# Kernel tuning notes

Hardware: AMD Instinct MI355X
Metric: run time of the kernel (lower is better)

## Reference

```python
import jax, jax.numpy as jnp
import numpy as np

L, B, T, E, NH, HD, HID, V = 8, 2, 2048, 1024, 16, 64, 2816, 32000


def _rmsnorm(x, w, eps=1e-6):
    return w * (x * jax.lax.rsqrt(jnp.mean(x * x, axis=-1, keepdims=True) + eps))


def _rope(x, cos, sin):
    # x: [B,H,T,D]; cos/sin: [1,1,T,D/2]
    x1, x2 = jnp.split(x, 2, axis=-1)
    return jnp.concatenate([x1 * cos - x2 * sin, x1 * sin + x2 * cos], axis=-1)


def setup_inputs() -> dict:
    key = jax.random.key(0)
    ks = jax.random.split(key, 7)
    s = 0.02
    return {
        "idx": jax.random.randint(ks[0], (B, T), 0, V),
        "tok_emb": jax.random.normal(ks[1], (V, E), dtype=jnp.float32) * s,
        "qkv_w": jax.random.normal(ks[2], (L, 3 * E, E), dtype=jnp.float32) * s,
        "proj_w": jax.random.normal(ks[3], (L, E, E), dtype=jnp.float32) * s,
        "w1": jax.random.normal(ks[4], (L, HID, E), dtype=jnp.float32) * s,
        "w2": jax.random.normal(ks[5], (L, HID, E), dtype=jnp.float32) * s,
        "w3": jax.random.normal(ks[6], (L, E, HID), dtype=jnp.float32) * s,
        "norm1_w": jnp.ones((L, E), dtype=jnp.float32),
        "norm2_w": jnp.ones((L, E), dtype=jnp.float32),
        "norm_f_w": jnp.ones((E,), dtype=jnp.float32),
    }


def reference(idx, tok_emb, qkv_w, proj_w, w1, w2, w3, norm1_w, norm2_w, norm_f_w):
    x = tok_emb[idx]  # [B,T,E]
    # RoPE cache (start_pos=0, no kv cache -> prefill path)
    half = HD // 2
    inv_freq = 1.0 / (10000.0 ** (jnp.arange(half, dtype=jnp.float32) / half))
    pos = jnp.arange(T, dtype=jnp.float32)
    freqs = pos[:, None] * inv_freq[None, :]  # [T, D/2]
    cos = jnp.cos(freqs)[None, None]
    sin = jnp.sin(freqs)[None, None]
    causal = jnp.tril(jnp.ones((T, T), dtype=bool))
    scale = 1.0 / np.sqrt(HD).astype(np.float32)

    for l in range(L):
        # attention block
        h = _rmsnorm(x, norm1_w[l])
        qkv = h @ qkv_w[l].T  # [B,T,3E]
        q, k, v = jnp.split(qkv, 3, axis=-1)
        q = q.reshape(B, T, NH, HD).transpose(0, 2, 1, 3)
        k = k.reshape(B, T, NH, HD).transpose(0, 2, 1, 3)
        v = v.reshape(B, T, NH, HD).transpose(0, 2, 1, 3)
        q = _rope(q, cos, sin)
        k = _rope(k, cos, sin)
        att = jnp.einsum('bhqd,bhkd->bhqk', q, k) * scale
        att = jnp.where(causal, att, -jnp.inf)
        att = jax.nn.softmax(att, axis=-1)
        o = jnp.einsum('bhqk,bhkd->bhqd', att, v)
        o = o.transpose(0, 2, 1, 3).reshape(B, T, E)
        x = x + o @ proj_w[l].T
        # SwiGLU MLP
        h = _rmsnorm(x, norm2_w[l])
        x = x + (jax.nn.silu(h @ w1[l].T) * (h @ w2[l].T)) @ w3[l].T

    x = _rmsnorm(x, norm_f_w)
    logits = x @ tok_emb.T  # tied lm_head
    return logits
```

## Files before the change

### kernel.cpp

```cpp
#include <hip/hip_runtime.h>

#define GLOBAL_AS __attribute__((address_space(1)))
#define LDS_AS __attribute__((address_space(3)))

typedef unsigned short u16;
typedef unsigned int u32;
typedef __attribute__((ext_vector_type(4))) float f32x4;
typedef __attribute__((ext_vector_type(8))) short bf16x8;

#define TT 2048
#define EE 1024
#define NHH 16
#define HDD 64
#define HIDD 2816
#define VV 32000
#define MM 4096

__device__ __forceinline__ u16 f2bf(float f) {
  u32 u = __builtin_bit_cast(u32, f);
  u += 0x7fffu + ((u >> 16) & 1u);
  return (u16)(u >> 16);
}
__device__ __forceinline__ float bf2f(u16 v) {
  return __builtin_bit_cast(float, (u32)v << 16);
}


__global__ __launch_bounds__(256) void castbf_k(const float* __restrict__ in,
                                                u16* __restrict__ o, long n4) {
  const long i = (long)blockIdx.x * 256 + threadIdx.x;
  if (i >= n4) return;
  const float4 v = ((const float4*)in)[i];
  ((uint2*)o)[i] = make_uint2((u32)f2bf(v.x) | ((u32)f2bf(v.y) << 16),
                              (u32)f2bf(v.z) | ((u32)f2bf(v.w) << 16));
}

__global__ void ropetab_k(float* __restrict__ cosT, float* __restrict__ sinT) {
  const int t = blockIdx.x, j = threadIdx.x;
  const float inv = powf(10000.0f, -(float)j * (1.0f / 32.0f));
  const float f = (float)t * inv;
  cosT[t * 32 + j] = cosf(f);
  sinT[t * 32 + j] = sinf(f);
}

__global__ __launch_bounds__(256) void embed_k(const int* __restrict__ idx,
                                               const float* __restrict__ temb,
                                               float* __restrict__ x) {
  const int row = blockIdx.x;
  const int id = idx[row];
  ((float4*)(x + (size_t)row * EE))[threadIdx.x] =
      ((const float4*)(temb + (size_t)id * EE))[threadIdx.x];
}

__global__ __launch_bounds__(256) void rmsnorm_k(const float* __restrict__ x,
                                                 const float* __restrict__ w,
                                                 u16* __restrict__ o) {
  __shared__ float red[4];
  const int row = blockIdx.x, tid = threadIdx.x;
  const float4 v = ((const float4*)(x + (size_t)row * EE))[tid];
  float ss = v.x * v.x + v.y * v.y + v.z * v.z + v.w * v.w;
#pragma unroll
  for (int off = 32; off; off >>= 1) ss += __shfl_xor(ss, off, 64);
  if ((tid & 63) == 0) red[tid >> 6] = ss;
  __syncthreads();
  const float inv = rsqrtf((red[0] + red[1] + red[2] + red[3]) * (1.0f / 1024.0f) + 1e-6f);
  const float4 wv = ((const float4*)w)[tid];
  const u32 lo = (u32)f2bf(v.x * inv * wv.x) | ((u32)f2bf(v.y * inv * wv.y) << 16);
  const u32 hi = (u32)f2bf(v.z * inv * wv.z) | ((u32)f2bf(v.w * inv * wv.w) << 16);
  ((uint2*)(o + (size_t)row * EE))[tid] = make_uint2(lo, hi);
}

template <int OUTBF>
__global__ __launch_bounds__(512, 2) void gemm256p(const u16* __restrict__ A,
                                                   const u16* __restrict__ Bw,
                                                   float* __restrict__ C,
                                                   u16* __restrict__ C16,
                                                   const u16* __restrict__ G,
                                                   const float* __restrict__ cosT,
                                                   const float* __restrict__ sinT,
                                                   u16* __restrict__ Qb,
                                                   u16* __restrict__ Kb,
                                                   u16* __restrict__ Vtb,
                                                   int N, int K) {
  __shared__ u16 lds[2 * 32768];
  const int t = threadIdx.x;
  const int lane = t & 63;
  const int wid = t >> 6;
  const int wr = wid >> 2;
  const int wc = wid & 3;
  const int l15 = lane & 15, lg = lane >> 4;
  const int bid = blockIdx.x;
  const int row0 = (bid & 15) << 8;
  const int col0 = (bid >> 4) << 8;
  const int NT = K >> 6;

  const int sr = t >> 3;
  const int su8 = (((t & 7) ^ (sr & 7)) << 3);
  const int t8 = t << 3;
  const u16* aG[4];
#pragma unroll
  for (int ga = 0; ga < 4; ++ga)
    aG[ga] = A + (size_t)(row0 + ga * 64 + sr) * K + su8;
  const u16* bG[4];
#pragma unroll
  for (int gb = 0; gb < 4; ++gb) {
    const int q = (gb * 2 + (sr >> 5)) & 3;
    const int nh = gb >> 1;
    bG[gb] = Bw + (size_t)(col0 + q * 64 + nh * 32 + (sr & 31)) * K + su8;
  }

  const int u0 = ((lg ^ (l15 & 7)) << 3);
  const int u1 = (((4 | lg) ^ (l15 & 7)) << 3);
  const int arow = (wr * 128 + l15) << 6;
  const int brow = 16384 + ((wc * 32 + l15) << 6);

  f32x4 acc[8][4] = {};

#define STA(nb, ga, k0n)                                                              \
  __builtin_amdgcn_global_load_lds((const GLOBAL_AS void*)(aG[ga] + (k0n)),           \
                                   (LDS_AS void*)((nb) + (ga)*4096 + t8), 16, 0, 0)
#define STB(nb, gb, k0n)                                                              \
  __builtin_amdgcn_global_load_lds((const GLOBAL_AS void*)(bG[gb] + (k0n)),           \
                                   (LDS_AS void*)((nb) + 16384 + (gb)*4096 + t8), 16, 0, 0)

  {
    u16* nb = lds;
    STA(nb, 0, 0); STA(nb, 2, 0);
    STB(nb, 0, 0); STB(nb, 1, 0);
    STB(nb, 2, 0); STB(nb, 3, 0);
    STA(nb, 1, 0); STA(nb, 3, 0);
  }

  bf16x8 af[4][2], bl[2][2], bh[2][2];

  for (int kt = 0; kt < NT; ++kt) {
    const bool st = (kt + 1 < NT);
    const int k0n = (kt + 1) << 6;
    const u16* cb = lds + (kt & 1) * 32768;
    u16* nb = lds + ((kt + 1) & 1) * 32768;

    asm volatile("s_waitcnt vmcnt(4)" ::: "memory");
    __builtin_amdgcn_s_barrier();
#pragma unroll
    for (int mi = 0; mi < 4; ++mi) {
      af[mi][0] = *(const bf16x8*)&cb[arow + mi * 1024 + u0];
      af[mi][1] = *(const bf16x8*)&cb[arow + mi * 1024 + u1];
    }
#pragma unroll
    for (int ni = 0; ni < 2; ++ni) {
      bl[ni][0] = *(const bf16x8*)&cb[brow + ni * 1024 + u0];
      bl[ni][1] = *(const bf16x8*)&cb[brow + ni * 1024 + u1];
    }
    if (st) { STA(nb, 0, k0n); STA(nb, 2, k0n); }
    __builtin_amdgcn_s_setprio(1);
#pragma unroll
    for (int mi = 0; mi < 4; ++mi)
#pragma unroll
      for (int ni = 0; ni < 2; ++ni) {
        acc[mi][ni] = __builtin_amdgcn_mfma_f32_16x16x32_bf16(af[mi][0], bl[ni][0], acc[mi][ni], 0, 0, 0);
        acc[mi][ni] = __builtin_amdgcn_mfma_f32_16x16x32_bf16(af[mi][1], bl[ni][1], acc[mi][ni], 0, 0, 0);
      }
    __builtin_amdgcn_s_setprio(0);

    if (st) { asm volatile("s_waitcnt vmcnt(4)" ::: "memory"); }
    else    { asm volatile("s_waitcnt vmcnt(2)" ::: "memory"); }
    __builtin_amdgcn_s_barrier();
#pragma unroll
    for (int ni = 0; ni < 2; ++ni) {
      bh[ni][0] = *(const bf16x8*)&cb[brow + 8192 + ni * 1024 + u0];
      bh[ni][1] = *(const bf16x8*)&cb[brow + 8192 + ni * 1024 + u1];
    }
    if (st) { STB(nb, 0, k0n); STB(nb, 1, k0n); }
    __builtin_amdgcn_s_setprio(1);
#pragma unroll
    for (int mi = 0; mi < 4; ++mi)
#pragma unroll
      for (int ni = 0; ni < 2; ++ni) {
        acc[mi][2 + ni] = __builtin_amdgcn_mfma_f32_16x16x32_bf16(af[mi][0], bh[ni][0], acc[mi][2 + ni], 0, 0, 0);
        acc[mi][2 + ni] = __builtin_amdgcn_mfma_f32_16x16x32_bf16(af[mi][1], bh[ni][1], acc[mi][2 + ni], 0, 0, 0);
      }
    __builtin_amdgcn_s_setprio(0);

    if (st) { asm volatile("s_waitcnt vmcnt(4)" ::: "memory"); }
    else    { asm volatile("s_waitcnt vmcnt(0)" ::: "memory"); }
    __builtin_amdgcn_s_barrier();
#pragma unroll
    for (int mi = 0; mi < 4; ++mi) {
      af[mi][0] = *(const bf16x8*)&cb[arow + (4 + mi) * 1024 + u0];
      af[mi][1] = *(const bf16x8*)&cb[arow + (4 + mi) * 1024 + u1];
    }
    if (st) { STB(nb, 2, k0n); STB(nb, 3, k0n); }
    __builtin_amdgcn_s_setprio(1);
#pragma unroll
    for (int mi = 0; mi < 4; ++mi)
#pragma unroll
      for (int ni = 0; ni < 2; ++ni) {
        acc[4 + mi][2 + ni] = __builtin_amdgcn_mfma_f32_16x16x32_bf16(af[mi][0], bh[ni][0], acc[4 + mi][2 + ni], 0, 0, 0);
        acc[4 + mi][2 + ni] = __builtin_amdgcn_mfma_f32_16x16x32_bf16(af[mi][1], bh[ni][1], acc[4 + mi][2 + ni], 0, 0, 0);
      }
    __builtin_amdgcn_s_setprio(0);

    if (st) { STA(nb, 1, k0n); STA(nb, 3, k0n); }
    __builtin_amdgcn_s_setprio(1);
#pragma unroll
    for (int mi = 0; mi < 4; ++mi)
#pragma unroll
      for (int ni = 0; ni < 2; ++ni) {
        acc[4 + mi][ni] = __builtin_amdgcn_mfma_f32_16x16x32_bf16(af[mi][0], bl[ni][0], acc[4 + mi][ni], 0, 0, 0);
        acc[4 + mi][ni] = __builtin_amdgcn_mfma_f32_16x16x32_bf16(af[mi][1], bl[ni][1], acc[4 + mi][ni], 0, 0, 0);
      }
    __builtin_amdgcn_s_setprio(0);
  }
#undef STA
#undef STB

  if (OUTBF == 3) {
    const int reg = col0 >> 10;
    const int fb = col0 & 1023;
#pragma unroll
    for (int m = 0; m < 8; ++m) {
      const int row = row0 + wr * 128 + m * 16 + lg * 4;
      const int b = row >> 11, tbase = row & 2047;
      if (reg < 2) {
        u16* dstp = (reg == 0) ? Qb : Kb;
        const float qs = (reg == 0) ? 0.125f : 1.0f;
#pragma unroll
        for (int n = 0; n < 2; ++n) {
          const int f = fb + wc * 64 + n * 16 + l15;
          const int h = f >> 6, j = f & 63;
#pragma unroll
          for (int r = 0; r < 4; ++r) {
            const int tt = tbase + r;
            const float c = cosT[tt * 32 + j], s = sinT[tt * 32 + j];
            const float x1 = acc[m][n][r], x2 = acc[m][n | 2][r];
            const size_t ro = ((size_t)(b * NHH + h) * TT + tt) * HDD + j;
            dstp[ro] = f2bf((x1 * c - x2 * s) * qs);
            dstp[ro + 32] = f2bf((x1 * s + x2 * c) * qs);
          }
        }
      } else {
#pragma unroll
        for (int n = 0; n < 4; ++n) {
          const int f = fb + wc * 64 + n * 16 + l15;
          const int h = f >> 6, j = f & 63;
          ushort4 pk;
          pk.x = f2bf(acc[m][n][0]);
          pk.y = f2bf(acc[m][n][1]);
          pk.z = f2bf(acc[m][n][2]);
          pk.w = f2bf(acc[m][n][3]);
          *(ushort4*)&Vtb[((size_t)(b * NHH + h) * HDD + j) * TT + tbase] = pk;
        }
      }
    }
    return;
  }

#pragma unroll
  for (int m = 0; m < 8; ++m) {
    const int row = row0 + wr * 128 + m * 16 + lg * 4;
#pragma unroll
    for (int n = 0; n < 4; ++n) {
      const int col = col0 + wc * 64 + n * 16 + l15;
#pragma unroll
      for (int r = 0; r < 4; ++r) {
        const size_t o = (size_t)(row + r) * N + col;
        if (OUTBF == 0) {
          C[o] = acc[m][n][r];
        } else if (OUTBF == 1) {
          C16[o] = f2bf(acc[m][n][r]);
        } else {
          const float g = bf2f(G[o]);
          C16[o] = f2bf(g / (1.0f + __expf(-g)) * acc[m][n][r]);
        }
      }
    }
  }
}

__global__ __launch_bounds__(512, 2) void gemm128r(const u16* __restrict__ A,
                                                   const u16* __restrict__ Bw,
                                                   float* __restrict__ C,
                                                   const float* __restrict__ R,
                                                   int N, int K) {
  __shared__ u16 lds[4 * 8192];
  const int t = threadIdx.x;
  const int lane = t & 63;
  const int wid = t >> 6;
  const int wr = wid >> 2;
  const int wc = wid & 3;
  const int l15 = lane & 15, lg = lane >> 4;
  const int bid = blockIdx.x;
  const int row0 = (bid & 31) << 7;
  const int col0 = (bid >> 5) << 7;
  const int NT = K >> 5;

  const int rA = t >> 2;
  const int usw = (((t & 3) ^ ((t >> 3) & 3)) << 3);
  const u16* sA = A + (size_t)(row0 + rA) * K + usw;
  const u16* sB = Bw + (size_t)(col0 + rA) * K + usw;
  const int dst = t << 3;

  const int e8 = ((lg ^ ((l15 >> 1) & 3)) << 3);
  const int aoff = (wr * 64 + l15) * 32 + e8;
  const int boff = 4096 + (wc * 32 + l15) * 32 + e8;

  f32x4 acc[4][2] = {};

  auto stage = [&](int kt) {
    u16* base = &lds[(kt & 3) * 8192];
    const size_t ko = (size_t)kt * 32;
    __builtin_amdgcn_global_load_lds((const GLOBAL_AS void*)(sA + ko),
                                     (LDS_AS void*)(base + dst), 16, 0, 0);
    __builtin_amdgcn_global_load_lds((const GLOBAL_AS void*)(sB + ko),
                                     (LDS_AS void*)(base + 4096 + dst), 16, 0, 0);
  };

  stage(0);
  stage(1);
  stage(2);

  for (int kt = 0; kt < NT; ++kt) {
    const int rem = NT - 1 - kt;
    if (rem >= 2) {
      asm volatile("s_waitcnt vmcnt(4)" ::: "memory");
    } else if (rem == 1) {
      asm volatile("s_waitcnt vmcnt(2)" ::: "memory");
    } else {
      asm volatile("s_waitcnt vmcnt(0)" ::: "memory");
    }
    __builtin_amdgcn_s_barrier();
    if (kt + 3 < NT) stage(kt + 3);
    const u16* base = &lds[(kt & 3) * 8192];
    bf16x8 af[4], bfv[2];
#pragma unroll
    for (int m = 0; m < 4; ++m) af[m] = *(const bf16x8*)&base[aoff + m * 512];
#pragma unroll
    for (int n = 0; n < 2; ++n) bfv[n] = *(const bf16x8*)&base[boff + n * 512];
    __builtin_amdgcn_s_setprio(1);
#pragma unroll
    for (int m = 0; m < 4; ++m)
#pragma unroll
      for (int n = 0; n < 2; ++n)
        acc[m][n] = __builtin_amdgcn_mfma_f32_16x16x32_bf16(af[m], bfv[n], acc[m][n], 0, 0, 0);
    __builtin_amdgcn_s_setprio(0);
  }

#pragma unroll
  for (int m = 0; m < 4; ++m) {
    const int row = row0 + wr * 64 + m * 16 + lg * 4;
#pragma unroll
    for (int n = 0; n < 2; ++n) {
      const int col = col0 + wc * 32 + n * 16 + l15;
#pragma unroll
      for (int r = 0; r < 4; ++r) {
        const size_t o = (size_t)(row + r) * N + col;
        C[o] = acc[m][n][r] + R[o];
      }
    }
  }
}

__global__ __launch_bounds__(256) void attn_k(const u16* __restrict__ Q,
                                              const u16* __restrict__ Kc,
                                              const u16* __restrict__ Vt,
                                              u16* __restrict__ O) {
  __shared__ u16 P_lds[4][32][72];
  const int bh = blockIdx.y;
  const int q0 = blockIdx.x * 128;
  const int lane = threadIdx.x & 63;
  const int w = threadIdx.x >> 6;
  const int l15 = lane & 15, lg = lane >> 4;
  const int qbase = q0 + w * 32;

  bf16x8 qf[2][2];
#pragma unroll
  for (int am = 0; am < 2; ++am)
#pragma unroll
    for (int ks = 0; ks < 2; ++ks)
      qf[am][ks] = *(const bf16x8*)&Q[((size_t)bh * TT + qbase + am * 16 + l15) * HDD + ks * 32 + lg * 8];

  bf16x8 ones;
#pragma unroll
  for (int i = 0; i < 8; ++i) ones[i] = (short)0x3F80;

  f32x4 oacc[2][4] = {};
  f32x4 lacc[2] = {};

  const int ntile = (q0 + 128) >> 6;
  for (int kt = 0; kt < ntile; ++kt) {
    const int k0 = kt << 6;
    f32x4 s[2][4];
    bf16x8 kf0[4], kf1[4];
#pragma unroll
    for (int an = 0; an < 4; ++an) {
      kf0[an] = *(const bf16x8*)&Kc[((size_t)bh * TT + k0 + an * 16 + l15) * HDD + lg * 8];
      kf1[an] = *(const bf16x8*)&Kc[((size_t)bh * TT + k0 + an * 16 + l15) * HDD + 32 + lg * 8];
    }
    __builtin_amdgcn_s_setprio(1);
#pragma unroll
    for (int an = 0; an < 4; ++an) {
#pragma unroll
      for (int am = 0; am < 2; ++am) {
        f32x4 z = {0.0f, 0.0f, 0.0f, 0.0f};
        z = __builtin_amdgcn_mfma_f32_16x16x32_bf16(qf[am][0], kf0[an], z, 0, 0, 0);
        s[am][an] = __builtin_amdgcn_mfma_f32_16x16x32_bf16(qf[am][1], kf1[an], z, 0, 0, 0);
      }
    }
    __builtin_amdgcn_s_setprio(0);
    const bool diag = (k0 + 64) > q0;
#pragma unroll
    for (int am = 0; am < 2; ++am)
#pragma unroll
      for (int an = 0; an < 4; ++an)
#pragma unroll
        for (int r = 0; r < 4; ++r) {
          float v = s[am][an][r];
          if (diag) {
            const int qrow = qbase + am * 16 + lg * 4 + r;
            const int kcol = k0 + an * 16 + l15;
            if (kcol > qrow) v = -1e30f;
          }
          s[am][an][r] = __expf(v);
        }
#pragma unroll
    for (int am = 0; am < 2; ++am)
#pragma unroll
      for (int an = 0; an < 4; ++an)
#pragma unroll
        for (int r = 0; r < 4; ++r)
          P_lds[w][am * 16 + lg * 4 + r][an * 16 + l15] = f2bf(s[am][an][r]);
#pragma unroll
    for (int ks = 0; ks < 2; ++ks) {
      bf16x8 pf[2];
#pragma unroll
      for (int am = 0; am < 2; ++am)
        pf[am] = *(const bf16x8*)&P_lds[w][am * 16 + l15][ks * 32 + lg * 8];
      __builtin_amdgcn_s_setprio(1);
#pragma unroll
      for (int dn = 0; dn < 4; ++dn) {
        const bf16x8 vf = *(const bf16x8*)&Vt[((size_t)bh * HDD + dn * 16 + l15) * TT + k0 + ks * 32 + lg * 8];
#pragma unroll
        for (int am = 0; am < 2; ++am)
          oacc[am][dn] = __builtin_amdgcn_mfma_f32_16x16x32_bf16(pf[am], vf, oacc[am][dn], 0, 0, 0);
      }
#pragma unroll
      for (int am = 0; am < 2; ++am)
        lacc[am] = __builtin_amdgcn_mfma_f32_16x16x32_bf16(pf[am], ones, lacc[am], 0, 0, 0);
      __builtin_amdgcn_s_setprio(0);
    }
  }
  const int b = bh >> 4, h = bh & 15;
#pragma unroll
  for (int am = 0; am < 2; ++am)
#pragma unroll
    for (int r = 0; r < 4; ++r) {
      const float il = 1.0f / lacc[am][r];
      const int qrow = qbase + am * 16 + lg * 4 + r;
#pragma unroll
      for (int dn = 0; dn < 4; ++dn)
        O[((size_t)b * TT + qrow) * EE + h * 64 + dn * 16 + l15] = f2bf(oacc[am][dn][r] * il);
    }
}


extern "C" void kernel_launch(void* const* d_in, const int* in_sizes, int n_in,
                              void* d_out, int out_size, void* d_ws, size_t ws_size,
                              hipStream_t stream) {
  const int* idx = (const int*)d_in[0];
  const float* tok_emb = (const float*)d_in[1];
  const float* qkv_w = (const float*)d_in[2];
  const float* proj_w = (const float*)d_in[3];
  const float* w1 = (const float*)d_in[4];
  const float* w2 = (const float*)d_in[5];
  const float* w3 = (const float*)d_in[6];
  const float* norm1_w = (const float*)d_in[7];
  const float* norm2_w = (const float*)d_in[8];
  const float* norm_f_w = (const float*)d_in[9];
  float* out = (float*)d_out;

  char* ws = (char*)d_ws;
  size_t off = 0;
  auto alloc = [&](size_t bytes) -> void* {
    off = (off + 255) & ~(size_t)255;
    void* p = ws + off;
    off += bytes;
    return p;
  };

  const size_t N_TEMB = (size_t)VV * EE;
  const size_t N_QKVW = (size_t)8 * 3 * EE * EE;
  const size_t N_PROJW = (size_t)8 * EE * EE;
  const size_t N_W1 = (size_t)8 * HIDD * EE;
  const size_t N_W3 = (size_t)8 * EE * HIDD;

  u16* tembbf = (u16*)alloc(N_TEMB * 2);
  u16* qkvwbf = (u16*)alloc(N_QKVW * 2);
  u16* projwbf = (u16*)alloc(N_PROJW * 2);
  u16* w1bf = (u16*)alloc(N_W1 * 2);
  u16* w2bf = (u16*)alloc(N_W1 * 2);
  u16* w3bf = (u16*)alloc(N_W3 * 2);
  float* x = (float*)alloc((size_t)MM * EE * 4);
  u16* h1 = (u16*)alloc((size_t)MM * EE * 2);
  u16* hg = (u16*)alloc((size_t)MM * HIDD * 2);
  u16* qb = (u16*)alloc((size_t)2 * NHH * TT * HDD * 2);
  u16* kb = (u16*)alloc((size_t)2 * NHH * TT * HDD * 2);
  u16* vtb = (u16*)alloc((size_t)2 * NHH * TT * HDD * 2);
  u16* attno = (u16*)alloc((size_t)MM * EE * 2);
  float* cosT = (float*)alloc((size_t)TT * 32 * 4);
  float* sinT = (float*)alloc((size_t)TT * 32 * 4);

  u16* g16 = (u16*)(out + 16777216);

  auto cast = [&](const float* src, u16* dst, size_t n) {
    const long n4 = (long)(n / 4);
    castbf_k<<<(int)((n4 + 255) / 256), 256, 0, stream>>>(src, dst, n4);
  };
  cast(tok_emb, tembbf, N_TEMB);
  cast(qkv_w, qkvwbf, N_QKVW);
  cast(proj_w, projwbf, N_PROJW);
  cast(w1, w1bf, N_W1);
  cast(w2, w2bf, N_W1);
  cast(w3, w3bf, N_W3);

  ropetab_k<<<TT, 32, 0, stream>>>(cosT, sinT);
  embed_k<<<MM, 256, 0, stream>>>(idx, tok_emb, x);

  for (int l = 0; l < 8; ++l) {
    rmsnorm_k<<<MM, 256, 0, stream>>>(x, norm1_w + l * EE, h1);
    gemm256p<3><<<dim3(12 * 16), 512, 0, stream>>>(h1, qkvwbf + (size_t)l * 3 * EE * EE,
                                                   nullptr, nullptr, nullptr,
                                                   cosT, sinT, qb, kb, vtb, 3 * EE, EE);
    attn_k<<<dim3(16, 32), 256, 0, stream>>>(qb, kb, vtb, attno);
    gemm128r<<<dim3(8 * 32), 512, 0, stream>>>(attno, projwbf + (size_t)l * EE * EE,
                                               x, x, EE, EE);
    rmsnorm_k<<<MM, 256, 0, stream>>>(x, norm2_w + l * EE, h1);
    gemm256p<1><<<dim3(11 * 16), 512, 0, stream>>>(h1, w1bf + (size_t)l * HIDD * EE,
                                                   nullptr, g16, nullptr,
                                                   nullptr, nullptr, nullptr, nullptr, nullptr,
                                                   HIDD, EE);
    gemm256p<2><<<dim3(11 * 16), 512, 0, stream>>>(h1, w2bf + (size_t)l * HIDD * EE,
                                                   nullptr, hg, g16,
                                                   nullptr, nullptr, nullptr, nullptr, nullptr,
                                                   HIDD, EE);
    gemm128r<<<dim3(8 * 32), 512, 0, stream>>>(hg, w3bf + (size_t)l * EE * HIDD,
                                               x, x, EE, HIDD);
  }
  rmsnorm_k<<<MM, 256, 0, stream>>>(x, norm_f_w, h1);
  gemm256p<0><<<dim3(125 * 16), 512, 0, stream>>>(h1, tembbf, out, nullptr, nullptr,
                                                  nullptr, nullptr, nullptr, nullptr, nullptr,
                                                  VV, EE);
}
```

Baseline: 2.741 ms.

## Move QKV and MLP GEMMs to 128x128 tiles and reorder attention blocks

Replaces the 256x256-tile GEMM for the QKV, w1 and w2 projections with a templated 128x128-tile kernel that carries the RoPE, SiLU-gate and residual epilogues, so these launches get many more workgroups (768/704 instead of 192/176). The proj and w3 residual GEMMs use the same kernel with a transposed wave layout. Attention becomes a 1D grid that pairs long and short causal query blocks, which should balance load across CUs. In exchange, smaller tiles lower arithmetic intensity and reuse per workgroup.

New measurement: 2.568 ms. 1.07x faster.

```diff
diff --git a/kernel.cpp b/kernel.cpp
--- a/kernel.cpp
+++ b/kernel.cpp
@@ -76,11 +76,6 @@
                                                    float* __restrict__ C,
                                                    u16* __restrict__ C16,
                                                    const u16* __restrict__ G,
-                                                   const float* __restrict__ cosT,
-                                                   const float* __restrict__ sinT,
-                                                   u16* __restrict__ Qb,
-                                                   u16* __restrict__ Kb,
-                                                   u16* __restrict__ Vtb,
                                                    int N, int K) {
   __shared__ u16 lds[2 * 32768];
   const int t = threadIdx.x;
@@ -214,12 +209,110 @@
 #undef STA
 #undef STB
 
+#pragma unroll
+  for (int m = 0; m < 8; ++m) {
+    const int row = row0 + wr * 128 + m * 16 + lg * 4;
+#pragma unroll
+    for (int n = 0; n < 4; ++n) {
+      const int col = col0 + wc * 64 + n * 16 + l15;
+#pragma unroll
+      for (int r = 0; r < 4; ++r) {
+        const size_t o = (size_t)(row + r) * N + col;
+        if (OUTBF == 0) {
+          C[o] = acc[m][n][r];
+        } else if (OUTBF == 1) {
+          C16[o] = f2bf(acc[m][n][r]);
+        } else {
+          const float g = bf2f(G[o]);
+          C16[o] = f2bf(g / (1.0f + __expf(-g)) * acc[m][n][r]);
+        }
+      }
+    }
+  }
+}
+
+template <int OUTBF>
+__global__ __launch_bounds__(512, 2) void gemm128n(const u16* __restrict__ A,
+                                                   const u16* __restrict__ Bw,
+                                                   float* __restrict__ C,
+                                                   const float* __restrict__ R,
+                                                   u16* __restrict__ C16,
+                                                   const u16* __restrict__ G,
+                                                   const float* __restrict__ cosT,
+                                                   const float* __restrict__ sinT,
+                                                   u16* __restrict__ Qb,
+                                                   u16* __restrict__ Kb,
+                                                   u16* __restrict__ Vtb,
+                                                   int N, int K) {
+  __shared__ u16 lds[4 * 8192];
+  const int t = threadIdx.x;
+  const int lane = t & 63;
+  const int wid = t >> 6;
+  const int wr = wid & 3;
+  const int wc = wid >> 2;
+  const int l15 = lane & 15, lg = lane >> 4;
+  const int bid = blockIdx.x;
+  const int row0 = (bid & 31) << 7;
+  const int col0 = (bid >> 5) << 7;
+  const int NT = K >> 5;
+
+  const int rA = t >> 2;
+  const int usw = (((t & 3) ^ ((t >> 3) & 3)) << 3);
+  const u16* sA = A + (size_t)(row0 + rA) * K + usw;
+  const u16* sB = Bw + (size_t)(col0 + rA) * K + usw;
+  const int dst = t << 3;
+
+  const int e8 = ((lg ^ ((l15 >> 1) & 3)) << 3);
+  const int aoff = (wr * 32 + l15) * 32 + e8;
+  const int boff = 4096 + (wc * 64 + l15) * 32 + e8;
+
+  f32x4 acc[2][4] = {};
+
+  auto stage = [&](int kt) {
+    u16* base = &lds[(kt & 3) * 8192];
+    const size_t ko = (size_t)kt * 32;
+    __builtin_amdgcn_global_load_lds((const GLOBAL_AS void*)(sA + ko),
+                                     (LDS_AS void*)(base + dst), 16, 0, 0);
+    __builtin_amdgcn_global_load_lds((const GLOBAL_AS void*)(sB + ko),
+                                     (LDS_AS void*)(base + 4096 + dst), 16, 0, 0);
+  };
+
+  stage(0);
+  stage(1);
+  stage(2);
+
+  for (int kt = 0; kt < NT; ++kt) {
+    const int rem = NT - 1 - kt;
+    if (rem >= 2) {
+      asm volatile("s_waitcnt vmcnt(4)" ::: "memory");
+    } else if (rem == 1) {
+      asm volatile("s_waitcnt vmcnt(2)" ::: "memory");
+    } else {
+      asm volatile("s_waitcnt vmcnt(0)" ::: "memory");
+    }
+    __builtin_amdgcn_s_barrier();
+    if (kt + 3 < NT) stage(kt + 3);
+    const u16* base = &lds[(kt & 3) * 8192];
+    bf16x8 af[2], bfv[4];
+#pragma unroll
+    for (int m = 0; m < 2; ++m) af[m] = *(const bf16x8*)&base[aoff + m * 512];
+#pragma unroll
+    for (int n = 0; n < 4; ++n) bfv[n] = *(const bf16x8*)&base[boff + n * 512];
+    __builtin_amdgcn_s_setprio(1);
+#pragma unroll
+    for (int m = 0; m < 2; ++m)
+#pragma unroll
+      for (int n = 0; n < 4; ++n)
+        acc[m][n] = __builtin_amdgcn_mfma_f32_16x16x32_bf16(af[m], bfv[n], acc[m][n], 0, 0, 0);
+    __builtin_amdgcn_s_setprio(0);
+  }
+
   if (OUTBF == 3) {
     const int reg = col0 >> 10;
     const int fb = col0 & 1023;
 #pragma unroll
-    for (int m = 0; m < 8; ++m) {
-      const int row = row0 + wr * 128 + m * 16 + lg * 4;
+    for (int m = 0; m < 2; ++m) {
+      const int row = row0 + wr * 32 + m * 16 + lg * 4;
       const int b = row >> 11, tbase = row & 2047;
       if (reg < 2) {
         u16* dstp = (reg == 0) ? Qb : Kb;
@@ -256,8 +349,8 @@
   }
 
 #pragma unroll
-  for (int m = 0; m < 8; ++m) {
-    const int row = row0 + wr * 128 + m * 16 + lg * 4;
+  for (int m = 0; m < 2; ++m) {
+    const int row = row0 + wr * 32 + m * 16 + lg * 4;
 #pragma unroll
     for (int n = 0; n < 4; ++n) {
       const int col = col0 + wc * 64 + n * 16 + l15;
@@ -265,7 +358,7 @@
       for (int r = 0; r < 4; ++r) {
         const size_t o = (size_t)(row + r) * N + col;
         if (OUTBF == 0) {
-          C[o] = acc[m][n][r];
+          C[o] = acc[m][n][r] + R[o];
         } else if (OUTBF == 1) {
           C16[o] = f2bf(acc[m][n][r]);
         } else {
@@ -277,96 +370,16 @@
   }
 }
 
-__global__ __launch_bounds__(512, 2) void gemm128r(const u16* __restrict__ A,
-                                                   const u16* __restrict__ Bw,
-                                                   float* __restrict__ C,
-                                                   const float* __restrict__ R,
-                                                   int N, int K) {
-  __shared__ u16 lds[4 * 8192];
-  const int t = threadIdx.x;
-  const int lane = t & 63;
-  const int wid = t >> 6;
-  const int wr = wid >> 2;
-  const int wc = wid & 3;
-  const int l15 = lane & 15, lg = lane >> 4;
-  const int bid = blockIdx.x;
-  const int row0 = (bid & 31) << 7;
-  const int col0 = (bid >> 5) << 7;
-  const int NT = K >> 5;
-
-  const int rA = t >> 2;
-  const int usw = (((t & 3) ^ ((t >> 3) & 3)) << 3);
-  const u16* sA = A + (size_t)(row0 + rA) * K + usw;
-  const u16* sB = Bw + (size_t)(col0 + rA) * K + usw;
-  const int dst = t << 3;
-
-  const int e8 = ((lg ^ ((l15 >> 1) & 3)) << 3);
-  const int aoff = (wr * 64 + l15) * 32 + e8;
-  const int boff = 4096 + (wc * 32 + l15) * 32 + e8;
-
-  f32x4 acc[4][2] = {};
-
-  auto stage = [&](int kt) {
-    u16* base = &lds[(kt & 3) * 8192];
-    const size_t ko = (size_t)kt * 32;
-    __builtin_amdgcn_global_load_lds((const GLOBAL_AS void*)(sA + ko),
-                                     (LDS_AS void*)(base + dst), 16, 0, 0);
-    __builtin_amdgcn_global_load_lds((const GLOBAL_AS void*)(sB + ko),
-                                     (LDS_AS void*)(base + 4096 + dst), 16, 0, 0);
-  };
-
-  stage(0);
-  stage(1);
-  stage(2);
-
-  for (int kt = 0; kt < NT; ++kt) {
-    const int rem = NT - 1 - kt;
-    if (rem >= 2) {
-      asm volatile("s_waitcnt vmcnt(4)" ::: "memory");
-    } else if (rem == 1) {
-      asm volatile("s_waitcnt vmcnt(2)" ::: "memory");
-    } else {
-      asm volatile("s_waitcnt vmcnt(0)" ::: "memory");
-    }
-    __builtin_amdgcn_s_barrier();
-    if (kt + 3 < NT) stage(kt + 3);
-    const u16* base = &lds[(kt & 3) * 8192];
-    bf16x8 af[4], bfv[2];
-#pragma unroll
-    for (int m = 0; m < 4; ++m) af[m] = *(const bf16x8*)&base[aoff + m * 512];
-#pragma unroll
-    for (int n = 0; n < 2; ++n) bfv[n] = *(const bf16x8*)&base[boff + n * 512];
-    __builtin_amdgcn_s_setprio(1);
-#pragma unroll
-    for (int m = 0; m < 4; ++m)
-#pragma unroll
-      for (int n = 0; n < 2; ++n)
-        acc[m][n] = __builtin_amdgcn_mfma_f32_16x16x32_bf16(af[m], bfv[n], acc[m][n], 0, 0, 0);
-    __builtin_amdgcn_s_setprio(0);
-  }
-
-#pragma unroll
-  for (int m = 0; m < 4; ++m) {
-    const int row = row0 + wr * 64 + m * 16 + lg * 4;
-#pragma unroll
-    for (int n = 0; n < 2; ++n) {
-      const int col = col0 + wc * 32 + n * 16 + l15;
-#pragma unroll
-      for (int r = 0; r < 4; ++r) {
-        const size_t o = (size_t)(row + r) * N + col;
-        C[o] = acc[m][n][r] + R[o];
-      }
-    }
-  }
-}
-
 __global__ __launch_bounds__(256) void attn_k(const u16* __restrict__ Q,
                                               const u16* __restrict__ Kc,
                                               const u16* __restrict__ Vt,
                                               u16* __restrict__ O) {
   __shared__ u16 P_lds[4][32][72];
-  const int bh = blockIdx.y;
-  const int q0 = blockIdx.x * 128;
+  const int bid = blockIdx.x;
+  const int bh = bid & 31;
+  const int jj = bid >> 5;
+  const int qi = (bid < 256) ? jj : 23 - jj;
+  const int q0 = qi << 7;
   const int lane = threadIdx.x & 63;
   const int w = threadIdx.x >> 6;
   const int l15 = lane & 15, lg = lane >> 4;
@@ -527,26 +540,29 @@
 
   for (int l = 0; l < 8; ++l) {
     rmsnorm_k<<<MM, 256, 0, stream>>>(x, norm1_w + l * EE, h1);
-    gemm256p<3><<<dim3(12 * 16), 512, 0, stream>>>(h1, qkvwbf + (size_t)l * 3 * EE * EE,
-                                                   nullptr, nullptr, nullptr,
+    gemm128n<3><<<dim3(24 * 32), 512, 0, stream>>>(h1, qkvwbf + (size_t)l * 3 * EE * EE,
+                                                   nullptr, nullptr, nullptr, nullptr,
                                                    cosT, sinT, qb, kb, vtb, 3 * EE, EE);
-    attn_k<<<dim3(16, 32), 256, 0, stream>>>(qb, kb, vtb, attno);
-    gemm128r<<<dim3(8 * 32), 512, 0, stream>>>(attno, projwbf + (size_t)l * EE * EE,
-                                               x, x, EE, EE);
+    attn_k<<<dim3(512), 256, 0, stream>>>(qb, kb, vtb, attno);
+    gemm128n<0><<<dim3(8 * 32), 512, 0, stream>>>(attno, projwbf + (size_t)l * EE * EE,
+                                                  x, x, nullptr, nullptr,
+                                                  nullptr, nullptr, nullptr, nullptr, nullptr,
+                                                  EE, EE);
     rmsnorm_k<<<MM, 256, 0, stream>>>(x, norm2_w + l * EE, h1);
-    gemm256p<1><<<dim3(11 * 16), 512, 0, stream>>>(h1, w1bf + (size_t)l * HIDD * EE,
-                                                   nullptr, g16, nullptr,
+    gemm128n<1><<<dim3(22 * 32), 512, 0, stream>>>(h1, w1bf + (size_t)l * HIDD * EE,
+                                                   nullptr, nullptr, g16, nullptr,
                                                    nullptr, nullptr, nullptr, nullptr, nullptr,
                                                    HIDD, EE);
-    gemm256p<2><<<dim3(11 * 16), 512, 0, stream>>>(h1, w2bf + (size_t)l * HIDD * EE,
-                                                   nullptr, hg, g16,
+    gemm128n<2><<<dim3(22 * 32), 512, 0, stream>>>(h1, w2bf + (size_t)l * HIDD * EE,
+                                                   nullptr, nullptr, hg, g16,
                                                    nullptr, nullptr, nullptr, nullptr, nullptr,
                                                    HIDD, EE);
-    gemm128r<<<dim3(8 * 32), 512, 0, stream>>>(hg, w3bf + (size_t)l * EE * HIDD,
-                                               x, x, EE, HIDD);
+    gemm128n<0><<<dim3(8 * 32), 512, 0, stream>>>(hg, w3bf + (size_t)l * EE * HIDD,
+                                                  x, x, nullptr, nullptr,
+                                                  nullptr, nullptr, nullptr, nullptr, nullptr,
+                                                  EE, HIDD);
   }
   rmsnorm_k<<<MM, 256, 0, stream>>>(x, norm_f_w, h1);
   gemm256p<0><<<dim3(125 * 16), 512, 0, stream>>>(h1, tembbf, out, nullptr, nullptr,
-                                                  nullptr, nullptr, nullptr, nullptr, nullptr,
                                                   VV, EE);
 }
```
